# Performance work log

Measured on AMD Instinct MI355X. Metric: run time of the kernel, lower is better.

Reference implementation:

```python
import jax, jax.numpy as jnp
import numpy as np

LN_EPS = 1e-5

def _layer_norm(x):
    m = jnp.mean(x, axis=-1, keepdims=True)
    v = jnp.mean(jnp.square(x - m), axis=-1, keepdims=True)
    return (x - m) / jnp.sqrt(v + LN_EPS)

def setup_inputs() -> dict:
    key = jax.random.key(0)
    ks = jax.random.split(key, 6)
    B, S, d_in, d_out = 8, 2048, 1024, 4096
    x = jax.random.normal(ks[0], (B, S, d_in), dtype=jnp.float32)
    # torch.randn % 1 -> values in [0, 1)
    weight_in = jax.random.uniform(ks[1], (d_out, d_in), dtype=jnp.float32)
    bias_in = jax.random.uniform(ks[2], (d_out,), dtype=jnp.float32)
    weight_out = jax.random.uniform(ks[3], (d_in, d_out), dtype=jnp.float32)
    bias_out = jax.random.uniform(ks[4], (d_in,), dtype=jnp.float32)
    lengths = jax.random.randint(ks[5], (B,), 1, S + 1, dtype=jnp.int64 if jax.config.read('jax_enable_x64') else jnp.int32)
    return {"x": x, "weight_in": weight_in, "bias_in": bias_in,
            "weight_out": weight_out, "bias_out": bias_out, "lengths": lengths}

def reference(x, weight_in, bias_in, weight_out, bias_out, lengths):
    # lengths is unused mathematically in the dense baseline (ragged kernels
    # only skip padded rows; valid-region math identical).
    for _ in range(10):
        x = jnp.einsum('bsd,od->bso', x, weight_in) + bias_in  # [B,S,d_out]
        x = _layer_norm(x)
        x = jnp.einsum('bso,do->bsd', x, weight_out) + bias_out  # [B,S,d_in]
        x = _layer_norm(x)
    return x
```

## Files before the change

kernel.cpp:

```cpp
#include <hip/hip_runtime.h>


typedef __attribute__((ext_vector_type(4))) float    f32x4;
typedef __attribute__((ext_vector_type(8))) _Float16 f16x8;
typedef __attribute__((ext_vector_type(4))) _Float16 f16x4;
typedef __attribute__((ext_vector_type(4))) uint     u32x4;

#define LN_EPS 1e-5f

__device__ __forceinline__ ushort f2h_bits(float f) {
    union { _Float16 h; ushort u; } c; c.h = (_Float16)f; return c.u;
}

typedef const __attribute__((address_space(1))) void* gas_ptr;
typedef __attribute__((address_space(3))) void* las_ptr;

__device__ __forceinline__ void gload_lds16(const void* g, void* l) {
    __builtin_amdgcn_global_load_lds((gas_ptr)g, (las_ptr)l, 16, 0, 0);
}

__device__ __forceinline__ f16x8 ldf(const _Float16* base, int byteoff) {
    return *reinterpret_cast<const f16x8*>(
        reinterpret_cast<const char*>(base) + byteoff);
}

__global__ __launch_bounds__(256) void conv_f32_f16(
        const float* __restrict__ in, _Float16* __restrict__ outp, int n4) {
    int i = blockIdx.x * 256 + threadIdx.x;
    if (i >= n4) return;
    float4 f = reinterpret_cast<const float4*>(in)[i];
    f16x4 r;
    r[0] = (_Float16)f.x; r[1] = (_Float16)f.y;
    r[2] = (_Float16)f.z; r[3] = (_Float16)f.w;
    *reinterpret_cast<f16x4*>(&outp[(size_t)i * 4]) = r;
}

template<int W>
__global__ __launch_bounds__(256)
void rowsum_rows(const _Float16* __restrict__ w, float* __restrict__ outp) {
    const int wid  = threadIdx.x >> 6;
    const int lane = threadIdx.x & 63;
    const size_t row = (size_t)blockIdx.x * 4 + wid;
    const _Float16* p = w + row * W;
    float s = 0.f;
    #pragma unroll
    for (int i = 0; i < W / 512; ++i) {
        f16x8 v = *reinterpret_cast<const f16x8*>(p + i * 512 + lane * 8);
        #pragma unroll
        for (int j = 0; j < 8; ++j) s += (float)v[j];
    }
    #pragma unroll
    for (int off = 32; off > 0; off >>= 1) s += __shfl_xor(s, off);
    if (lane == 0) outp[row] = s;
}

template<int M, int N, int K, bool FIRST>
__global__ __launch_bounds__(512)
void gemm256_ln(const _Float16* __restrict__ A, const _Float16* __restrict__ B,
                const float* __restrict__ bias, const float* __restrict__ wsum,
                const float2* __restrict__ pin, _Float16* __restrict__ C,
                float2* __restrict__ partials) {
    constexpr int NT   = K / 64;
    constexpr int NIT  = NT / 2;
    constexpr int NBX  = N / 256;
    constexpr int NWG  = (M / 256) * NBX;
    constexpr int NPIN = K / 256;

    __shared__ __attribute__((aligned(16))) _Float16 lds[2][2][2][8192];

    const int tid  = threadIdx.x;
    const int wid  = tid >> 6;
    const int lane = tid & 63;
    const int wr   = wid >> 2;
    const int wc   = wid & 3;

    int bn0, bm0;
    if constexpr (NBX == 16) {
        const int x = blockIdx.x & 7, j = blockIdx.x >> 3;
        bn0 = (x * 2 + (j & 1)) * 256;
        bm0 = (j >> 1) * 256;
    } else {
        int bid = (blockIdx.x & 7) * (NWG >> 3) + (blockIdx.x >> 3);
        bn0 = (bid % NBX) * 256;
        bm0 = (bid / NBX) * 256;
    }

    const int trow = tid >> 3;
    const int cg   = (tid & 7) ^ (trow & 7);
    const _Float16* Asrc = A + (size_t)(bm0 + trow) * K + cg * 8;
    const _Float16* Bsrc = B + (size_t)(bn0 + trow) * K + cg * 8;

    const int fr  = lane & 15;
    const int fq  = lane >> 4;
    const int s8  = lane & 7;
    const int cb0 = ((fq       ^ s8) << 4);
    const int cb1 = (((4 + fq) ^ s8) << 4);
    const int brb = (wc & 1) * 64;

    const _Float16* Ah[2] = { &lds[0][0][wr][0],      &lds[1][0][wr][0] };
    const _Float16* Bh[2] = { &lds[0][1][wc >> 1][0], &lds[1][1][wc >> 1][0] };

    f32x4 acc[8][4] = {};
    f16x8 aLo[4][2], aHi[4][2], bLo[2][2], bHi[2][2];

#define STAGE_A(buf, h, kk) do { \
    gload_lds16(Asrc + (size_t)((h)*128     ) * K + (kk), (void*)&lds[buf][0][h][       wid*512]); \
    gload_lds16(Asrc + (size_t)((h)*128 + 64) * K + (kk), (void*)&lds[buf][0][h][4096 + wid*512]); } while(0)
#define STAGE_B(buf, h, kk) do { \
    gload_lds16(Bsrc + (size_t)((h)*128     ) * K + (kk), (void*)&lds[buf][1][h][       wid*512]); \
    gload_lds16(Bsrc + (size_t)((h)*128 + 64) * K + (kk), (void*)&lds[buf][1][h][4096 + wid*512]); } while(0)

#define READ_ALO(b) do { _Pragma("unroll") for (int i = 0; i < 4; ++i) { \
    aLo[i][0] = ldf(Ah[b], (i*16+fr)*128 + cb0); \
    aLo[i][1] = ldf(Ah[b], (i*16+fr)*128 + cb1); } } while(0)
#define READ_AHI(b) do { _Pragma("unroll") for (int i = 0; i < 4; ++i) { \
    aHi[i][0] = ldf(Ah[b], ((i+4)*16+fr)*128 + cb0); \
    aHi[i][1] = ldf(Ah[b], ((i+4)*16+fr)*128 + cb1); } } while(0)
#define READ_BLO(b) do { _Pragma("unroll") for (int j = 0; j < 2; ++j) { \
    bLo[j][0] = ldf(Bh[b], (brb + j*16 + fr)*128 + cb0); \
    bLo[j][1] = ldf(Bh[b], (brb + j*16 + fr)*128 + cb1); } } while(0)
#define READ_BHI(b) do { _Pragma("unroll") for (int j = 0; j < 2; ++j) { \
    bHi[j][0] = ldf(Bh[b], (brb + (j+2)*16 + fr)*128 + cb0); \
    bHi[j][1] = ldf(Bh[b], (brb + (j+2)*16 + fr)*128 + cb1); } } while(0)

#define MFMA_BLK(AF, ioff, BF, joff) do { \
    _Pragma("unroll") for (int i = 0; i < 4; ++i) \
    _Pragma("unroll") for (int j = 0; j < 2; ++j) { \
        acc[i+ioff][j+joff] = __builtin_amdgcn_mfma_f32_16x16x32_f16(AF[i][0], BF[j][0], acc[i+ioff][j+joff], 0, 0, 0); \
        acc[i+ioff][j+joff] = __builtin_amdgcn_mfma_f32_16x16x32_f16(AF[i][1], BF[j][1], acc[i+ioff][j+joff], 0, 0, 0); } } while(0)

#define BARRIER() __builtin_amdgcn_s_barrier()
#define VMCNT4()  asm volatile("s_waitcnt vmcnt(4)" ::: "memory")

    STAGE_B(0, 0, 0);  STAGE_B(0, 1, 0);
    STAGE_A(0, 0, 0);  STAGE_A(0, 1, 0);
    STAGE_B(1, 0, 64); STAGE_B(1, 1, 64);
    VMCNT4();
    BARRIER();

    float bcol[4], wcol[4];
    #pragma unroll
    for (int j = 0; j < 4; ++j) {
        const int c = bn0 + wc * 64 + j * 16 + fr;
        bcol[j] = bias[c]; wcol[j] = wsum[c];
    }

    for (int it = 0; it < NIT; ++it) {
        const int k1 = it * 128 + 64;
        const int k2 = (it * 128 + 128) & (K - 1);
        const int k3 = (it * 128 + 192) & (K - 1);

        READ_ALO(0); READ_BLO(0);
        STAGE_A(1, 0, k1);
        BARRIER();
        __builtin_amdgcn_s_setprio(1); MFMA_BLK(aLo, 0, bLo, 0); __builtin_amdgcn_s_setprio(0);
        BARRIER();
        READ_BHI(0);
        STAGE_A(1, 1, k1);
        BARRIER();
        __builtin_amdgcn_s_setprio(1); MFMA_BLK(aLo, 0, bHi, 2); __builtin_amdgcn_s_setprio(0);
        BARRIER();
        READ_AHI(0);
        STAGE_B(0, 0, k2);
        BARRIER();
        __builtin_amdgcn_s_setprio(1); MFMA_BLK(aHi, 4, bLo, 0); __builtin_amdgcn_s_setprio(0);
        BARRIER();
        STAGE_B(0, 1, k2);
        BARRIER();
        __builtin_amdgcn_s_setprio(1); MFMA_BLK(aHi, 4, bHi, 2); __builtin_amdgcn_s_setprio(0);
        VMCNT4();
        BARRIER();
        READ_ALO(1); READ_BLO(1);
        STAGE_A(0, 0, k2);
        BARRIER();
        __builtin_amdgcn_s_setprio(1); MFMA_BLK(aLo, 0, bLo, 0); __builtin_amdgcn_s_setprio(0);
        BARRIER();
        READ_BHI(1);
        STAGE_A(0, 1, k2);
        BARRIER();
        __builtin_amdgcn_s_setprio(1); MFMA_BLK(aLo, 0, bHi, 2); __builtin_amdgcn_s_setprio(0);
        BARRIER();
        READ_AHI(1);
        STAGE_B(1, 0, k3);
        BARRIER();
        __builtin_amdgcn_s_setprio(1); MFMA_BLK(aHi, 4, bLo, 0); __builtin_amdgcn_s_setprio(0);
        BARRIER();
        STAGE_B(1, 1, k3);
        BARRIER();
        __builtin_amdgcn_s_setprio(1); MFMA_BLK(aHi, 4, bHi, 2); __builtin_amdgcn_s_setprio(0);
        VMCNT4();
        BARRIER();
    }

    float2* sst = (float2*)&lds[0][0][0][0];
    if constexpr (FIRST) {
        if (tid < 256) sst[tid] = make_float2(0.f, 1.f);
    } else {
        const int row  = tid >> 1;
        const int half = tid & 1;
        const float2* pr = pin + (size_t)(bm0 + row) * NPIN + half * (NPIN / 2);
        float s = 0.f, q = 0.f;
        #pragma unroll
        for (int k = 0; k < NPIN / 2; ++k) { s += pr[k].x; q += pr[k].y; }
        s += __shfl_xor(s, 1); q += __shfl_xor(q, 1);
        if (half == 0) {
            const float mean = s * (1.0f / K);
            const float var  = fmaxf(q * (1.0f / K) - mean * mean, 0.f);
            sst[row] = make_float2(mean, rsqrtf(var + LN_EPS));
        }
    }
    __syncthreads();

    ushort* eps = (ushort*)&lds[1][0][0][0];
    #pragma unroll
    for (int pass = 0; pass < 4; ++pass) {
        if (wr == (pass >> 1)) {
            #pragma unroll
            for (int i2 = 0; i2 < 4; ++i2) {
                const int i = (pass & 1) * 4 + i2;
                #pragma unroll
                for (int q = 0; q < 4; ++q) {
                    const int rloc = wr * 128 + i * 16 + fq * 4 + q;
                    const int rl   = rloc - pass * 64;
                    const float2 st = sst[rloc];
                    const float rs = st.y, coef = st.y * st.x;
                    const int key = ((rl >> 2) & 3) << 4;
                    #pragma unroll
                    for (int j = 0; j < 4; ++j) {
                        const float v = rs * acc[i][j][q] - coef * wcol[j] + bcol[j];
                        const int c = wc * 64 + j * 16 + fr;
                        eps[rl * 256 + (c ^ key)] = f2h_bits(v);
                    }
                }
            }
        }
        BARRIER();
        {
            const int rl  = tid >> 3;
            const int a8  = tid & 7;
            const int r   = bm0 + pass * 64 + rl;
            const int key = ((rl >> 2) & 3) << 4;
            float s = 0.f, sq = 0.f;
            ushort* crow = (ushort*)(C + (size_t)r * N + bn0);
            #pragma unroll
            for (int k = 0; k < 4; ++k) {
                const int ch = 8 * k + a8;
                u32x4 d = *reinterpret_cast<const u32x4*>(&eps[rl * 256 + ch * 8]);
                const f16x8 v = *reinterpret_cast<const f16x8*>(&d);
                #pragma unroll
                for (int e = 0; e < 8; ++e) {
                    const float f = (float)v[e];
                    s += f; sq += f * f;
                }
                *reinterpret_cast<u32x4*>(&crow[(ch * 8) ^ key]) = d;
            }
            s  += __shfl_xor(s, 1);  sq += __shfl_xor(sq, 1);
            s  += __shfl_xor(s, 2);  sq += __shfl_xor(sq, 2);
            s  += __shfl_xor(s, 4);  sq += __shfl_xor(sq, 4);
            if (a8 == 0)
                partials[(size_t)r * NBX + (bn0 >> 8)] = make_float2(s, sq);
        }
        BARRIER();
    }
#undef STAGE_A
#undef STAGE_B
#undef READ_ALO
#undef READ_AHI
#undef READ_BLO
#undef READ_BHI
#undef MFMA_BLK
#undef BARRIER
#undef VMCNT4
}

__global__ __launch_bounds__(256)
void ln_final(const _Float16* __restrict__ a, const float2* __restrict__ part,
              float* __restrict__ outp) {
    const int wid  = threadIdx.x >> 6;
    const int lane = threadIdx.x & 63;
    const size_t row = (size_t)blockIdx.x * 4 + wid;

    float s = 0.f, q = 0.f;
    if (lane < 4) { const float2 p = part[row * 4 + lane]; s = p.x; q = p.y; }
    s += __shfl_xor(s, 1); q += __shfl_xor(q, 1);
    s += __shfl_xor(s, 2); q += __shfl_xor(q, 2);
    s = __shfl(s, 0); q = __shfl(q, 0);
    const float mean = s * (1.0f / 1024.f);
    const float var  = fmaxf(q * (1.0f / 1024.f) - mean * mean, 0.f);
    const float rstd = rsqrtf(var + LN_EPS);

    const _Float16* p = a + row * 1024;
    #pragma unroll
    for (int i = 0; i < 2; ++i) {
        f16x8 v = *reinterpret_cast<const f16x8*>(p + i * 512 + lane * 8);
        float* op = outp + row * 1024 + i * 512 + lane * 8;
        float4 o0, o1;
        o0.x = ((float)v[0] - mean) * rstd;
        o0.y = ((float)v[1] - mean) * rstd;
        o0.z = ((float)v[2] - mean) * rstd;
        o0.w = ((float)v[3] - mean) * rstd;
        o1.x = ((float)v[4] - mean) * rstd;
        o1.y = ((float)v[5] - mean) * rstd;
        o1.z = ((float)v[6] - mean) * rstd;
        o1.w = ((float)v[7] - mean) * rstd;
        reinterpret_cast<float4*>(op)[0] = o0;
        reinterpret_cast<float4*>(op)[1] = o1;
    }
}

extern "C" void kernel_launch(void* const* d_in, const int* in_sizes, int n_in,
                              void* d_out, int out_size, void* d_ws, size_t ws_size,
                              hipStream_t stream) {
    const float* x     = (const float*)d_in[0];
    const float* w_in  = (const float*)d_in[1];
    const float* b_in  = (const float*)d_in[2];
    const float* w_out = (const float*)d_in[3];
    const float* b_out = (const float*)d_in[4];

    constexpr int Mrows = 16384;
    constexpr int Din   = 1024;
    constexpr int Dout  = 4096;

    char* ws = (char*)d_ws;
    _Float16* wib = (_Float16*)ws; ws += (size_t)Dout * Din * 2;
    _Float16* wob = (_Float16*)ws; ws += (size_t)Din * Dout * 2;
    _Float16* a2b = (_Float16*)ws; ws += (size_t)Mrows * Din * 2;
    _Float16* a1b = (_Float16*)ws; ws += (size_t)Mrows * Dout * 2;
    float* winsum  = (float*)ws;   ws += Dout * 4;
    float* woutsum = (float*)ws;   ws += Din * 4;
    float2* p1  = (float2*)ws;     ws += (size_t)Mrows * 16 * 8;
    float2* p2  = (float2*)ws;

    const dim3 blk(256);

    conv_f32_f16<<<(Dout * Din / 4) / 256, blk, 0, stream>>>(w_in,  wib, Dout * Din / 4);
    conv_f32_f16<<<(Din * Dout / 4) / 256, blk, 0, stream>>>(w_out, wob, Din * Dout / 4);
    conv_f32_f16<<<(Mrows * Din / 4) / 256, blk, 0, stream>>>(x, a2b, Mrows * Din / 4);
    rowsum_rows<Din> <<<Dout / 4, blk, 0, stream>>>(wib, winsum);
    rowsum_rows<Dout><<<Din / 4,  blk, 0, stream>>>(wob, woutsum);

    for (int it = 0; it < 10; ++it) {
        if (it == 0)
            gemm256_ln<Mrows, Dout, Din, true>
                <<<(Mrows / 256) * (Dout / 256), dim3(512), 0, stream>>>(
                    a2b, wib, b_in, winsum, p2, a1b, p1);
        else
            gemm256_ln<Mrows, Dout, Din, false>
                <<<(Mrows / 256) * (Dout / 256), dim3(512), 0, stream>>>(
                    a2b, wib, b_in, winsum, p2, a1b, p1);
        gemm256_ln<Mrows, Din, Dout, false>
            <<<(Mrows / 256) * (Din / 256), dim3(512), 0, stream>>>(
                a1b, wob, b_out, woutsum, p1, a2b, p2);
    }
    ln_final<<<Mrows / 4, blk, 0, stream>>>(a2b, p2, (float*)d_out);
}
```

Baseline: 2.778 ms.

## Make first GEMM persistent over four N tiles with a new tile-to-block mapping

The up-projection GEMM (1024 output tiles) now launches 256 workgroups, and each one loops over four consecutive 256-wide N tiles for the same M block. This removes tail-wave effects and launch overhead by matching the grid to the CU count. The down-projection keeps one tile per block but gets a new mapping from block index to tile, meant to improve L2 locality across XCDs. Each extra tile adds a full pipeline drain (vmcnt(0) plus a barrier) between tiles, and the LN row statistics are reloaded for every tile.

Result: slower. 4.637 ms (+66.9%).

```diff
diff --git a/kernel.cpp b/kernel.cpp
--- a/kernel.cpp
+++ b/kernel.cpp
@@ -54,7 +54,7 @@
     if (lane == 0) outp[row] = s;
 }
 
-template<int M, int N, int K, bool FIRST>
+template<int M, int N, int K, int NP, bool FIRST>
 __global__ __launch_bounds__(512)
 void gemm256_ln(const _Float16* __restrict__ A, const _Float16* __restrict__ B,
                 const float* __restrict__ bias, const float* __restrict__ wsum,
@@ -63,7 +63,6 @@
     constexpr int NT   = K / 64;
     constexpr int NIT  = NT / 2;
     constexpr int NBX  = N / 256;
-    constexpr int NWG  = (M / 256) * NBX;
     constexpr int NPIN = K / 256;
 
     __shared__ __attribute__((aligned(16))) _Float16 lds[2][2][2][8192];
@@ -74,21 +73,20 @@
     const int wr   = wid >> 2;
     const int wc   = wid & 3;
 
-    int bn0, bm0;
-    if constexpr (NBX == 16) {
+    int bn_base, bm0;
+    if constexpr (NP == 4) {
         const int x = blockIdx.x & 7, j = blockIdx.x >> 3;
-        bn0 = (x * 2 + (j & 1)) * 256;
-        bm0 = (j >> 1) * 256;
+        bn_base = (x >> 1) * 1024;
+        bm0     = ((x & 1) * 32 + j) * 256;
     } else {
-        int bid = (blockIdx.x & 7) * (NWG >> 3) + (blockIdx.x >> 3);
-        bn0 = (bid % NBX) * 256;
-        bm0 = (bid / NBX) * 256;
+        const int x = blockIdx.x & 7, j = blockIdx.x >> 3;
+        bn_base = (x >> 1) * 256;
+        bm0     = (j * 2 + (x & 1)) * 256;
     }
 
     const int trow = tid >> 3;
     const int cg   = (tid & 7) ^ (trow & 7);
     const _Float16* Asrc = A + (size_t)(bm0 + trow) * K + cg * 8;
-    const _Float16* Bsrc = B + (size_t)(bn0 + trow) * K + cg * 8;
 
     const int fr  = lane & 15;
     const int fq  = lane >> 4;
@@ -99,9 +97,6 @@
 
     const _Float16* Ah[2] = { &lds[0][0][wr][0],      &lds[1][0][wr][0] };
     const _Float16* Bh[2] = { &lds[0][1][wc >> 1][0], &lds[1][1][wc >> 1][0] };
-
-    f32x4 acc[8][4] = {};
-    f16x8 aLo[4][2], aHi[4][2], bLo[2][2], bHi[2][2];
 
 #define STAGE_A(buf, h, kk) do { \
     gload_lds16(Asrc + (size_t)((h)*128     ) * K + (kk), (void*)&lds[buf][0][h][       wid*512]); \
@@ -131,136 +126,147 @@
 
 #define BARRIER() __builtin_amdgcn_s_barrier()
 #define VMCNT4()  asm volatile("s_waitcnt vmcnt(4)" ::: "memory")
-
-    STAGE_B(0, 0, 0);  STAGE_B(0, 1, 0);
-    STAGE_A(0, 0, 0);  STAGE_A(0, 1, 0);
-    STAGE_B(1, 0, 64); STAGE_B(1, 1, 64);
-    VMCNT4();
-    BARRIER();
-
-    float bcol[4], wcol[4];
-    #pragma unroll
-    for (int j = 0; j < 4; ++j) {
-        const int c = bn0 + wc * 64 + j * 16 + fr;
-        bcol[j] = bias[c]; wcol[j] = wsum[c];
-    }
-
-    for (int it = 0; it < NIT; ++it) {
-        const int k1 = it * 128 + 64;
-        const int k2 = (it * 128 + 128) & (K - 1);
-        const int k3 = (it * 128 + 192) & (K - 1);
-
-        READ_ALO(0); READ_BLO(0);
-        STAGE_A(1, 0, k1);
-        BARRIER();
-        __builtin_amdgcn_s_setprio(1); MFMA_BLK(aLo, 0, bLo, 0); __builtin_amdgcn_s_setprio(0);
-        BARRIER();
-        READ_BHI(0);
-        STAGE_A(1, 1, k1);
-        BARRIER();
-        __builtin_amdgcn_s_setprio(1); MFMA_BLK(aLo, 0, bHi, 2); __builtin_amdgcn_s_setprio(0);
-        BARRIER();
-        READ_AHI(0);
-        STAGE_B(0, 0, k2);
-        BARRIER();
-        __builtin_amdgcn_s_setprio(1); MFMA_BLK(aHi, 4, bLo, 0); __builtin_amdgcn_s_setprio(0);
-        BARRIER();
-        STAGE_B(0, 1, k2);
-        BARRIER();
-        __builtin_amdgcn_s_setprio(1); MFMA_BLK(aHi, 4, bHi, 2); __builtin_amdgcn_s_setprio(0);
+#define VMCNT0()  asm volatile("s_waitcnt vmcnt(0)" ::: "memory")
+
+    for (int p = 0; p < NP; ++p) {
+        const int bn0 = bn_base + p * 256;
+        const _Float16* Bsrc = B + (size_t)(bn0 + trow) * K + cg * 8;
+
+        if (p) { VMCNT0(); BARRIER(); }
+
+        STAGE_B(0, 0, 0);  STAGE_B(0, 1, 0);
+        STAGE_A(0, 0, 0);  STAGE_A(0, 1, 0);
+        STAGE_B(1, 0, 64); STAGE_B(1, 1, 64);
         VMCNT4();
         BARRIER();
-        READ_ALO(1); READ_BLO(1);
-        STAGE_A(0, 0, k2);
-        BARRIER();
-        __builtin_amdgcn_s_setprio(1); MFMA_BLK(aLo, 0, bLo, 0); __builtin_amdgcn_s_setprio(0);
-        BARRIER();
-        READ_BHI(1);
-        STAGE_A(0, 1, k2);
-        BARRIER();
-        __builtin_amdgcn_s_setprio(1); MFMA_BLK(aLo, 0, bHi, 2); __builtin_amdgcn_s_setprio(0);
-        BARRIER();
-        READ_AHI(1);
-        STAGE_B(1, 0, k3);
-        BARRIER();
-        __builtin_amdgcn_s_setprio(1); MFMA_BLK(aHi, 4, bLo, 0); __builtin_amdgcn_s_setprio(0);
-        BARRIER();
-        STAGE_B(1, 1, k3);
-        BARRIER();
-        __builtin_amdgcn_s_setprio(1); MFMA_BLK(aHi, 4, bHi, 2); __builtin_amdgcn_s_setprio(0);
-        VMCNT4();
-        BARRIER();
-    }
-
-    float2* sst = (float2*)&lds[0][0][0][0];
-    if constexpr (FIRST) {
-        if (tid < 256) sst[tid] = make_float2(0.f, 1.f);
-    } else {
-        const int row  = tid >> 1;
-        const int half = tid & 1;
-        const float2* pr = pin + (size_t)(bm0 + row) * NPIN + half * (NPIN / 2);
-        float s = 0.f, q = 0.f;
+
+        f32x4 acc[8][4] = {};
+        f16x8 aLo[4][2], aHi[4][2], bLo[2][2], bHi[2][2];
+
+        for (int it = 0; it < NIT; ++it) {
+            const int k1 = it * 128 + 64;
+            const int k2 = (it * 128 + 128) & (K - 1);
+            const int k3 = (it * 128 + 192) & (K - 1);
+
+            READ_ALO(0); READ_BLO(0);
+            STAGE_A(1, 0, k1);
+            BARRIER();
+            __builtin_amdgcn_s_setprio(1); MFMA_BLK(aLo, 0, bLo, 0); __builtin_amdgcn_s_setprio(0);
+            BARRIER();
+            READ_BHI(0);
+            STAGE_A(1, 1, k1);
+            BARRIER();
+            __builtin_amdgcn_s_setprio(1); MFMA_BLK(aLo, 0, bHi, 2); __builtin_amdgcn_s_setprio(0);
+            BARRIER();
+            READ_AHI(0);
+            STAGE_B(0, 0, k2);
+            BARRIER();
+            __builtin_amdgcn_s_setprio(1); MFMA_BLK(aHi, 4, bLo, 0); __builtin_amdgcn_s_setprio(0);
+            BARRIER();
+            STAGE_B(0, 1, k2);
+            BARRIER();
+            __builtin_amdgcn_s_setprio(1); MFMA_BLK(aHi, 4, bHi, 2); __builtin_amdgcn_s_setprio(0);
+            VMCNT4();
+            BARRIER();
+            READ_ALO(1); READ_BLO(1);
+            STAGE_A(0, 0, k2);
+            BARRIER();
+            __builtin_amdgcn_s_setprio(1); MFMA_BLK(aLo, 0, bLo, 0); __builtin_amdgcn_s_setprio(0);
+            BARRIER();
+            READ_BHI(1);
+            STAGE_A(0, 1, k2);
+            BARRIER();
+            __builtin_amdgcn_s_setprio(1); MFMA_BLK(aLo, 0, bHi, 2); __builtin_amdgcn_s_setprio(0);
+            BARRIER();
+            READ_AHI(1);
+            STAGE_B(1, 0, k3);
+            BARRIER();
+            __builtin_amdgcn_s_setprio(1); MFMA_BLK(aHi, 4, bLo, 0); __builtin_amdgcn_s_setprio(0);
+            BARRIER();
+            STAGE_B(1, 1, k3);
+            BARRIER();
+            __builtin_amdgcn_s_setprio(1); MFMA_BLK(aHi, 4, bHi, 2); __builtin_amdgcn_s_setprio(0);
+            VMCNT4();
+            BARRIER();
+        }
+
+        float2* sst = (float2*)&lds[0][0][0][0];
+        if constexpr (FIRST) {
+            if (tid < 256) sst[tid] = make_float2(0.f, 1.f);
+        } else {
+            const int row  = tid >> 1;
+            const int half = tid & 1;
+            const float2* pr = pin + (size_t)(bm0 + row) * NPIN + half * (NPIN / 2);
+            float s = 0.f, q = 0.f;
+            #pragma unroll
+            for (int k = 0; k < NPIN / 2; ++k) { s += pr[k].x; q += pr[k].y; }
+            s += __shfl_xor(s, 1); q += __shfl_xor(q, 1);
+            if (half == 0) {
+                const float mean = s * (1.0f / K);
+                const float var  = fmaxf(q * (1.0f / K) - mean * mean, 0.f);
+                sst[row] = make_float2(mean, rsqrtf(var + LN_EPS));
+            }
+        }
+        __syncthreads();
+
+        float bcol[4], wcol[4];
         #pragma unroll
-        for (int k = 0; k < NPIN / 2; ++k) { s += pr[k].x; q += pr[k].y; }
-        s += __shfl_xor(s, 1); q += __shfl_xor(q, 1);
-        if (half == 0) {
-            const float mean = s * (1.0f / K);
-            const float var  = fmaxf(q * (1.0f / K) - mean * mean, 0.f);
-            sst[row] = make_float2(mean, rsqrtf(var + LN_EPS));
+        for (int j = 0; j < 4; ++j) {
+            const int c = bn0 + wc * 64 + j * 16 + fr;
+            bcol[j] = bias[c]; wcol[j] = wsum[c];
         }
-    }
-    __syncthreads();
-
-    ushort* eps = (ushort*)&lds[1][0][0][0];
-    #pragma unroll
-    for (int pass = 0; pass < 4; ++pass) {
-        if (wr == (pass >> 1)) {
-            #pragma unroll
-            for (int i2 = 0; i2 < 4; ++i2) {
-                const int i = (pass & 1) * 4 + i2;
+
+        ushort* eps = (ushort*)&lds[1][0][0][0];
+        #pragma unroll
+        for (int pass = 0; pass < 4; ++pass) {
+            if (wr == (pass >> 1)) {
                 #pragma unroll
-                for (int q = 0; q < 4; ++q) {
-                    const int rloc = wr * 128 + i * 16 + fq * 4 + q;
-                    const int rl   = rloc - pass * 64;
-                    const float2 st = sst[rloc];
-                    const float rs = st.y, coef = st.y * st.x;
-                    const int key = ((rl >> 2) & 3) << 4;
+                for (int i2 = 0; i2 < 4; ++i2) {
+                    const int i = (pass & 1) * 4 + i2;
                     #pragma unroll
-                    for (int j = 0; j < 4; ++j) {
-                        const float v = rs * acc[i][j][q] - coef * wcol[j] + bcol[j];
-                        const int c = wc * 64 + j * 16 + fr;
-                        eps[rl * 256 + (c ^ key)] = f2h_bits(v);
+                    for (int q = 0; q < 4; ++q) {
+                        const int rloc = wr * 128 + i * 16 + fq * 4 + q;
+                        const int rl   = rloc - pass * 64;
+                        const float2 st = sst[rloc];
+                        const float rs = st.y, coef = st.y * st.x;
+                        const int key = ((rl >> 2) & 3) << 4;
+                        #pragma unroll
+                        for (int j = 0; j < 4; ++j) {
+                            const float v = rs * acc[i][j][q] - coef * wcol[j] + bcol[j];
+                            const int c = wc * 64 + j * 16 + fr;
+                            eps[rl * 256 + (c ^ key)] = f2h_bits(v);
+                        }
                     }
                 }
             }
+            BARRIER();
+            {
+                const int rl  = tid >> 3;
+                const int a8  = tid & 7;
+                const int r   = bm0 + pass * 64 + rl;
+                const int key = ((rl >> 2) & 3) << 4;
+                float s = 0.f, sq = 0.f;
+                ushort* crow = (ushort*)(C + (size_t)r * N + bn0);
+                #pragma unroll
+                for (int k = 0; k < 4; ++k) {
+                    const int ch = 8 * k + a8;
+                    u32x4 d = *reinterpret_cast<const u32x4*>(&eps[rl * 256 + ch * 8]);
+                    const f16x8 v = *reinterpret_cast<const f16x8*>(&d);
+                    #pragma unroll
+                    for (int e = 0; e < 8; ++e) {
+                        const float f = (float)v[e];
+                        s += f; sq += f * f;
+                    }
+                    *reinterpret_cast<u32x4*>(&crow[(ch * 8) ^ key]) = d;
+                }
+                s  += __shfl_xor(s, 1);  sq += __shfl_xor(sq, 1);
+                s  += __shfl_xor(s, 2);  sq += __shfl_xor(sq, 2);
+                s  += __shfl_xor(s, 4);  sq += __shfl_xor(sq, 4);
+                if (a8 == 0)
+                    partials[(size_t)r * NBX + (bn0 >> 8)] = make_float2(s, sq);
+            }
+            BARRIER();
         }
-        BARRIER();
-        {
-            const int rl  = tid >> 3;
-            const int a8  = tid & 7;
-            const int r   = bm0 + pass * 64 + rl;
-            const int key = ((rl >> 2) & 3) << 4;
-            float s = 0.f, sq = 0.f;
-            ushort* crow = (ushort*)(C + (size_t)r * N + bn0);
-            #pragma unroll
-            for (int k = 0; k < 4; ++k) {
-                const int ch = 8 * k + a8;
-                u32x4 d = *reinterpret_cast<const u32x4*>(&eps[rl * 256 + ch * 8]);
-                const f16x8 v = *reinterpret_cast<const f16x8*>(&d);
-                #pragma unroll
-                for (int e = 0; e < 8; ++e) {
-                    const float f = (float)v[e];
-                    s += f; sq += f * f;
-                }
-                *reinterpret_cast<u32x4*>(&crow[(ch * 8) ^ key]) = d;
-            }
-            s  += __shfl_xor(s, 1);  sq += __shfl_xor(sq, 1);
-            s  += __shfl_xor(s, 2);  sq += __shfl_xor(sq, 2);
-            s  += __shfl_xor(s, 4);  sq += __shfl_xor(sq, 4);
-            if (a8 == 0)
-                partials[(size_t)r * NBX + (bn0 >> 8)] = make_float2(s, sq);
-        }
-        BARRIER();
     }
 #undef STAGE_A
 #undef STAGE_B
@@ -271,6 +277,7 @@
 #undef MFMA_BLK
 #undef BARRIER
 #undef VMCNT4
+#undef VMCNT0
 }
 
 __global__ __launch_bounds__(256)
@@ -341,16 +348,13 @@
 
     for (int it = 0; it < 10; ++it) {
         if (it == 0)
-            gemm256_ln<Mrows, Dout, Din, true>
-                <<<(Mrows / 256) * (Dout / 256), dim3(512), 0, stream>>>(
-                    a2b, wib, b_in, winsum, p2, a1b, p1);
+            gemm256_ln<Mrows, Dout, Din, 4, true>
+                <<<256, dim3(512), 0, stream>>>(a2b, wib, b_in, winsum, p2, a1b, p1);
         else
-            gemm256_ln<Mrows, Dout, Din, false>
-                <<<(Mrows / 256) * (Dout / 256), dim3(512), 0, stream>>>(
-                    a2b, wib, b_in, winsum, p2, a1b, p1);
-        gemm256_ln<Mrows, Din, Dout, false>
-            <<<(Mrows / 256) * (Din / 256), dim3(512), 0, stream>>>(
-                a1b, wob, b_out, woutsum, p1, a2b, p2);
+            gemm256_ln<Mrows, Dout, Din, 4, false>
+                <<<256, dim3(512), 0, stream>>>(a2b, wib, b_in, winsum, p2, a1b, p1);
+        gemm256_ln<Mrows, Din, Dout, 1, false>
+            <<<256, dim3(512), 0, stream>>>(a1b, wob, b_out, woutsum, p1, a2b, p2);
     }
     ln_final<<<Mrows / 4, blk, 0, stream>>>(a2b, p2, (float*)d_out);
 }
```
